# Kernel optimization log

Hardware: AMD Instinct MI355X
Metric: run time of the kernel (lower is better)

The kernel has to match this reference:

```python
import jax, jax.numpy as jnp
import numpy as np

B, N, KNN_K = 4, 4096, 32
C1, C = 128, 256
K_SLOTS, RECON_M, N_RECON = 4, 96, 128
SLOT_ITERS = 3

def _ln(x, g, b):
    m = x.mean(-1, keepdims=True)
    v = jnp.var(x, axis=-1, keepdims=True)
    return (x - m) * jax.lax.rsqrt(v + 1e-5) * g + b

def _gather(f, idx):
    # f [B,P,C], idx [B,N,K] -> [B,N,K,C]
    return jax.vmap(lambda a, i: a[i])(f, idx)

def _knn(xyz, k):
    sq = jnp.sum(xyz * xyz, -1)
    d = sq[:, :, None] + sq[:, None, :] - 2.0 * jnp.einsum('bnc,bmc->bnm', xyz, xyz)
    return jax.lax.top_k(-d, k)[1]

def _conv_block(xyz, feats, W, b):
    # InterZPConv-style: KNN neighbor gather -> per-neighbor transform -> max aggregate
    idx = _knn(xyz, KNN_K)
    rel = _gather(xyz, idx) - xyz[:, :, None, :]
    h = jnp.concatenate([_gather(feats, idx), rel], axis=-1)
    h = jax.nn.relu(jnp.einsum('bnkc,cd->bnkd', h, W) + b)
    return h.max(axis=2)

def _bn(x, g, b):
    # BatchNorm2d (training mode) over (batch, slot) axes for 1x1-conv stacks
    m = x.mean(axis=(0, 1), keepdims=True)
    v = jnp.var(x, axis=(0, 1), keepdims=True)
    return (x - m) * jax.lax.rsqrt(v + 1e-5) * g + b

def _gru(upd, prev, W_ih, W_hh, b_ih, b_hh):
    gi = upd @ W_ih + b_ih
    gh = prev @ W_hh + b_hh
    r = jax.nn.sigmoid(gi[..., :C] + gh[..., :C])
    z = jax.nn.sigmoid(gi[..., C:2 * C] + gh[..., C:2 * C])
    n = jnp.tanh(gi[..., 2 * C:] + r * gh[..., 2 * C:])
    return (1.0 - z) * n + z * prev

def _chamfer(a, b):
    # a [B,M,3], b [B,P,3] -> (min over b per a-point, min over a per b-point), squared dists
    d = jnp.sum((a[..., :, None, :] - b[..., None, :, :]) ** 2, axis=-1)
    return d.min(axis=-1), d.min(axis=-2)

def _fps(pts):
    # farthest point sampling of N_RECON points from pts [P,3]
    P = pts.shape[0]
    d0 = jnp.full((P,), 1e10, pts.dtype)
    def step(carry, _):
        d, last = carry
        d = jnp.minimum(d, jnp.sum((pts - pts[last]) ** 2, axis=-1))
        nxt = jnp.argmax(d).astype(jnp.int32)
        return (d, nxt), nxt
    _, idxs = jax.lax.scan(step, (d0, jnp.array(0, jnp.int32)), None, length=N_RECON - 1)
    return jnp.concatenate([jnp.zeros((1,), jnp.int32), idxs])

def setup_inputs() -> dict:
    key = jax.random.key(0)
    ks = jax.random.split(key, 16)
    w = lambda k, s: jax.random.normal(k, s, jnp.float32) * 0.02
    z = lambda *s: jnp.zeros(s, jnp.float32)
    o = lambda *s: jnp.ones(s, jnp.float32)
    return {
        'x': jax.random.normal(ks[0], (B, 3, N), jnp.float32),
        'pose': jnp.zeros((B, N, 4, 4), jnp.float32),
        'W1': w(ks[1], (1 + 3, C1)), 'b1': z(C1),
        'W2': w(ks[2], (C1 + 3, C)), 'b2': z(C),
        'slots_mu': w(ks[3], (1, 1, C)), 'slots_sigma': jnp.abs(w(ks[4], (1, 1, C))) + 0.01,
        'ln_in_g': o(C), 'ln_in_b': z(C),
        'ln_slot_g': o(C), 'ln_slot_b': z(C),
        'ln_ff_g': o(C), 'ln_ff_b': z(C),
        'Wq': w(ks[5], (C, C)), 'Wk': w(ks[6], (C, C)), 'Wv': w(ks[7], (C, C)),
        'W_ih': w(ks[8], (C, 3 * C)), 'W_hh': w(ks[9], (C, 3 * C)),
        'b_ih': z(3 * C), 'b_hh': z(3 * C),
        'Wm1': w(ks[10], (C, C)), 'bm1': z(C),
        'Wm2': w(ks[11], (C, C)), 'bm2': z(C),
        'Wr1': w(ks[12], (C, C)), 'br1': z(C), 'g1': o(C), 'be1': z(C),
        'Wr2': w(ks[13], (C, C)), 'br2': z(C), 'g2': o(C), 'be2': z(C),
        'Wr3': w(ks[14], (C, RECON_M * 3)), 'br3': z(RECON_M * 3),
    }

def reference(x, pose, W1, b1, W2, b2, slots_mu, slots_sigma, ln_in_g, ln_in_b,
              ln_slot_g, ln_slot_b, ln_ff_g, ln_ff_b, Wq, Wk, Wv,
              W_ih, W_hh, b_ih, b_hh, Wm1, bm1, Wm2, bm2,
              Wr1, br1, g1, be1, Wr2, br2, g2, be2, Wr3, br3):
    xyz = jnp.transpose(x, (0, 2, 1))  # [B,N,3]
    feats = jnp.ones((B, N, 1), x.dtype)  # preprocess_input: unit features, na=1
    f = _conv_block(xyz, feats, W1, b1)   # [B,N,C1]
    f = _conv_block(xyz, f, W2, b2)       # [B,N,C]
    # Slot attention over per-point invariant features
    inp = _ln(f, ln_in_g, ln_in_b)
    kk = inp @ Wk
    vv = inp @ Wv
    slots = slots_mu + slots_sigma * jax.random.normal(jax.random.key(42), (B, K_SLOTS, C), x.dtype)
    scale = C ** -0.5
    attn = None
    for _ in range(SLOT_ITERS):
        prev = slots
        q = _ln(slots, ln_slot_g, ln_slot_b) @ Wq
        logits = scale * jnp.einsum('bkc,bnc->bkn', q, kk)
        attn = jax.nn.softmax(logits, axis=1)  # softmax over slots
        wgt = attn / (attn.sum(axis=-1, keepdims=True) + 1e-8)
        upd = jnp.einsum('bkn,bnc->bkc', wgt, vv)
        slots = _gru(upd, prev, W_ih, W_hh, b_ih, b_hh)
        h = _ln(slots, ln_ff_g, ln_ff_b)
        slots = slots + (jax.nn.relu(h @ Wm1 + bm1) @ Wm2 + bm2)
    attn_out = jnp.transpose(attn, (0, 2, 1))  # [B,N,K] (attn_ori.transpose(1,2))
    # Part reconstruction net (1x1 conv + BN + ReLU stack on slot features)
    h = jax.nn.relu(_bn(slots @ Wr1 + br1, g1, be1))
    h = jax.nn.relu(_bn(h @ Wr2 + br2, g2, be2))
    slot_points = (h @ Wr3 + br3).reshape(B, K_SLOTS, RECON_M, 3)
    all_pts = slot_points.reshape(B, K_SLOTS * RECON_M, 3)
    # FPS downsample + global chamfer against input points
    idx = jax.vmap(_fps)(all_pts)  # [B, N_RECON]
    ds = jnp.take_along_axis(all_pts, idx[..., None], axis=1)  # [B,N_RECON,3]
    d1, d2 = _chamfer(ds, xyz)
    loss = (d1.mean(-1) + d2.mean(-1)).mean()
    return loss, attn_out
```

## Files before the change

### kernel.cpp

```cpp
#include <hip/hip_runtime.h>

#define NBATCH 4
#define NPTS   4096
#define KNNK   32
#define C1D    128
#define CD     256
#define KPAD   160
#define ASTR   168
#define ASTR2  264

typedef _Float16 v8h __attribute__((ext_vector_type(8)));
typedef float    v4f __attribute__((ext_vector_type(4)));
typedef unsigned long long ull;


__device__ __forceinline__ float block_sum256(float v, float* red) {
    #pragma unroll
    for (int o = 32; o; o >>= 1) v += __shfl_down(v, o);
    __syncthreads();
    if ((threadIdx.x & 63) == 0) red[threadIdx.x >> 6] = v;
    __syncthreads();
    return red[0] + red[1] + red[2] + red[3];
}

__device__ __forceinline__ unsigned rotl32(unsigned x, unsigned r) {
    return (x << r) | (x >> (32u - r));
}

__device__ float erfinv_f(float x) {
    float w = -log1pf(-x * x);
    float p;
    if (w < 5.0f) {
        w -= 2.5f;
        p = 2.81022636e-08f;
        p = fmaf(p, w, 3.43273939e-07f);
        p = fmaf(p, w, -3.5233877e-06f);
        p = fmaf(p, w, -4.39150654e-06f);
        p = fmaf(p, w, 0.00021858087f);
        p = fmaf(p, w, -0.00125372503f);
        p = fmaf(p, w, -0.00417768164f);
        p = fmaf(p, w, 0.246640727f);
        p = fmaf(p, w, 1.50140941f);
    } else {
        w = sqrtf(w) - 3.0f;
        p = -0.000200214257f;
        p = fmaf(p, w, 0.000100950558f);
        p = fmaf(p, w, 0.00134934322f);
        p = fmaf(p, w, -0.00367342844f);
        p = fmaf(p, w, 0.00573950773f);
        p = fmaf(p, w, -0.0076224613f);
        p = fmaf(p, w, 0.00943887047f);
        p = fmaf(p, w, 1.00167406f);
        p = fmaf(p, w, 2.83297682f);
    }
    return p * x;
}

__device__ __forceinline__ float bits_to_normal(unsigned bits) {
    unsigned fb = (bits >> 9) | 0x3f800000u;
    float f = __uint_as_float(fb) - 1.0f;
    const float lo = -0.99999994f;
    float u = fmaf(f, 2.0f, lo);
    u = fmaxf(u, lo);
    return 1.41421356237f * erfinv_f(u);
}

__device__ __forceinline__ unsigned fmap(float f) {
    unsigned b = __float_as_uint(f);
    return (b & 0x80000000u) ? ~b : (b | 0x80000000u);
}

template <int CTRL, int RM>
__device__ __forceinline__ ull dpp_min_u64(ull k) {
    unsigned lo = (unsigned)k, hi = (unsigned)(k >> 32);
    unsigned tlo = (unsigned)__builtin_amdgcn_update_dpp((int)lo, (int)lo, CTRL, RM, 0xf, false);
    unsigned thi = (unsigned)__builtin_amdgcn_update_dpp((int)hi, (int)hi, CTRL, RM, 0xf, false);
    ull t = ((ull)thi << 32) | tlo;
    return t < k ? t : k;
}

template <int CTRL, int RM>
__device__ __forceinline__ void dpp_lexmax(float& v, int& ix) {
    int tv = __builtin_amdgcn_update_dpp(__float_as_int(v), __float_as_int(v), CTRL, RM, 0xf, false);
    int ti = __builtin_amdgcn_update_dpp(ix, ix, CTRL, RM, 0xf, false);
    float fv = __int_as_float(tv);
    bool take = (fv > v) || (fv == v && ti < ix);
    v  = take ? fv : v;
    ix = take ? ti : ix;
}


__global__ __launch_bounds__(256) void prep_kernel(const float* __restrict__ x,
                                                   float* __restrict__ xyz,
                                                   float4* __restrict__ xyzw,
                                                   const float* __restrict__ mu,
                                                   const float* __restrict__ sg,
                                                   float* __restrict__ slots,
                                                   float* __restrict__ asum,
                                                   const float* __restrict__ W2,
                                                   const float* __restrict__ Wk,
                                                   const float* __restrict__ Wv,
                                                   _Float16* __restrict__ W2t,
                                                   _Float16* __restrict__ WkvT,
                                                   unsigned* __restrict__ counter) {
    int t = threadIdx.x;
    if (blockIdx.x < 64) {
        int gid = blockIdx.x * 256 + t;
        int b = gid >> 12, n = gid & (NPTS - 1);
        float a0 = x[(b * 3 + 0) * NPTS + n];
        float a1 = x[(b * 3 + 1) * NPTS + n];
        float a2 = x[(b * 3 + 2) * NPTS + n];
        xyz[gid * 3 + 0] = a0; xyz[gid * 3 + 1] = a1; xyz[gid * 3 + 2] = a2;
        float sq = a0 * a0 + a1 * a1 + a2 * a2;
        xyzw[gid] = make_float4(a0, a1, a2, sq);
        if (gid < 16) asum[gid] = 0.0f;
        if (gid == 16) counter[0] = 0u;
        if (gid < 2048) {
            int j = gid;
            unsigned ks0 = 0u, ks1 = 42u, ks2 = 0u ^ 42u ^ 0x1BD11BDAu;
            unsigned x0 = (unsigned)j + ks0;
            unsigned x1 = (unsigned)(j + 2048) + ks1;
            #define RND(r) { x0 += x1; x1 = rotl32(x1, r); x1 ^= x0; }
            RND(13u) RND(15u) RND(26u) RND(6u);  x0 += ks1; x1 += ks2 + 1u;
            RND(17u) RND(29u) RND(16u) RND(24u); x0 += ks2; x1 += ks0 + 2u;
            RND(13u) RND(15u) RND(26u) RND(6u);  x0 += ks0; x1 += ks1 + 3u;
            RND(17u) RND(29u) RND(16u) RND(24u); x0 += ks1; x1 += ks2 + 4u;
            RND(13u) RND(15u) RND(26u) RND(6u);  x0 += ks2; x1 += ks0 + 5u;
            #undef RND
            int c0 = j & 255, c1 = (j + 2048) & 255;
            slots[j]        = mu[c0] + sg[c0] * bits_to_normal(x0);
            slots[j + 2048] = mu[c1] + sg[c1] * bits_to_normal(x1);
        }
    } else if (blockIdx.x < 320) {
        int nb = blockIdx.x - 64;
        if (t < KPAD) W2t[nb * KPAD + t] = (t < 131) ? (_Float16)W2[t * CD + nb] : (_Float16)0.0f;
    } else {
        int n = blockIdx.x - 320;
        float v = (n < 256) ? Wk[t * CD + n] : Wv[t * CD + (n - 256)];
        WkvT[n * CD + t] = (_Float16)v;
    }
}

__global__ __launch_bounds__(256) void knn_kernel(const float4* __restrict__ xyzw,
                                                  int* __restrict__ knn_idx) {
    int wid = threadIdx.x >> 6, lane = threadIdx.x & 63;
    int pid = blockIdx.x * 4 + wid;
    int b = pid >> 12, n = pid & (NPTS - 1);
    const float4* xb = xyzw + (size_t)b * NPTS;
    float4 p = xb[n];
    unsigned d[64];
    #pragma unroll
    for (int i = 0; i < 64; ++i) {
        float4 c = xb[i * 64 + lane];
        float dot = p.x * c.x + p.y * c.y + p.z * c.z;
        d[i] = fmap(p.w + c.w - 2.0f * dot);
    }
    unsigned gv[8]; int gi[8];
    #pragma unroll
    for (int g = 0; g < 8; ++g) {
        unsigned mv = d[g * 8]; int mi = g * 8;
        #pragma unroll
        for (int j = 1; j < 8; ++j)
            if (d[g * 8 + j] < mv) { mv = d[g * 8 + j]; mi = g * 8 + j; }
        gv[g] = mv; gi[g] = mi * 64 + lane;
    }
    unsigned lv = gv[0]; int li = gi[0];
    #pragma unroll
    for (int g = 1; g < 8; ++g)
        if (gv[g] < lv) { lv = gv[g]; li = gi[g]; }

    int* out = knn_idx + (size_t)pid * KNNK;
    #pragma unroll 1
    for (int s = 0; s < KNNK; ++s) {
        ull k = ((ull)lv << 32) | (unsigned)li;
        k = dpp_min_u64<0x111, 0xf>(k);
        k = dpp_min_u64<0x112, 0xf>(k);
        k = dpp_min_u64<0x114, 0xf>(k);
        k = dpp_min_u64<0x118, 0xf>(k);
        k = dpp_min_u64<0x142, 0xa>(k);
        k = dpp_min_u64<0x143, 0xc>(k);
        int fm = __builtin_amdgcn_readlane((int)(unsigned)k, 63);
        if (lane == 0) out[s] = fm;
        int flane = fm & 63;
        int slot  = fm >> 6;
        if (lane == flane) {
            int g = slot >> 3;
            #pragma unroll
            for (int g2 = 0; g2 < 8; ++g2) {
                if (g2 == g) {
                    #pragma unroll
                    for (int j = 0; j < 8; ++j)
                        if (g2 * 8 + j == slot) d[g2 * 8 + j] = 0xFFFFFFFFu;
                    unsigned mv = d[g2 * 8]; int mi = g2 * 8;
                    #pragma unroll
                    for (int j = 1; j < 8; ++j)
                        if (d[g2 * 8 + j] < mv) { mv = d[g2 * 8 + j]; mi = g2 * 8 + j; }
                    gv[g2] = mv; gi[g2] = mi * 64 + lane;
                }
            }
            lv = gv[0]; li = gi[0];
            #pragma unroll
            for (int g2 = 1; g2 < 8; ++g2)
                if (gv[g2] < lv) { lv = gv[g2]; li = gi[g2]; }
        }
    }
}

__global__ __launch_bounds__(128) void conv1_kernel(const float* __restrict__ xyz,
                                                    const int* __restrict__ knn_idx,
                                                    const float* __restrict__ W1,
                                                    const float* __restrict__ b1,
                                                    _Float16* __restrict__ f1h) {
    int pid = blockIdx.x;
    int b = pid >> 12, n = pid & (NPTS - 1);
    int d = threadIdx.x, lane = threadIdx.x & 63;
    const float* xb = xyz + (size_t)b * NPTS * 3;
    float w0 = W1[d], wx = W1[C1D + d], wy = W1[2 * C1D + d], wz = W1[3 * C1D + d];
    float bb = b1[d];
    float px = xb[n * 3], py = xb[n * 3 + 1], pz = xb[n * 3 + 2];
    const int* idx = knn_idx + (size_t)pid * KNNK;
    float cx = 0.0f, cy = 0.0f, cz = 0.0f;
    if (lane < 32) {
        int j = idx[lane];
        cx = xb[j * 3]; cy = xb[j * 3 + 1]; cz = xb[j * 3 + 2];
    }
    float m = -1e30f;
    #pragma unroll
    for (int k = 0; k < KNNK; ++k) {
        float jx = __shfl(cx, k), jy = __shfl(cy, k), jz = __shfl(cz, k);
        float v = w0 + bb + (jx - px) * wx + (jy - py) * wy + (jz - pz) * wz;
        m = fmaxf(m, v);
    }
    f1h[(size_t)pid * C1D + d] = (_Float16)fmaxf(m, 0.0f);
}

__global__ __launch_bounds__(256) void conv2_mfma_kernel(const float* __restrict__ xyz,
                                                         const _Float16* __restrict__ f1h,
                                                         const int* __restrict__ knn_idx,
                                                         const _Float16* __restrict__ W2t,
                                                         const float* __restrict__ b2,
                                                         const float* __restrict__ g_in,
                                                         const float* __restrict__ b_in,
                                                         _Float16* __restrict__ inph) {
    __shared__ _Float16 A[64 * ASTR];
    __shared__ float colmax[2 * CD];
    __shared__ float red[4];
    int pid2 = blockIdx.x;
    int gp0 = pid2 * 2;
    int b = gp0 >> 12, n0 = gp0 & (NPTS - 1);
    int tid = threadIdx.x;
    const int* idx = knn_idx + (size_t)pid2 * 64;
    const float* xb = xyz + (size_t)b * NPTS * 3;

    {
        int r = tid & 63, seg = tid >> 6;
        int j = idx[r];
        const uint4* s4 = (const uint4*)(f1h + ((size_t)b * NPTS + j) * C1D);
        uint4* d4 = (uint4*)&A[r * ASTR];
        #pragma unroll
        for (int i = 0; i < 4; ++i) d4[seg * 4 + i] = s4[seg * 4 + i];
        unsigned* z = (unsigned*)&A[r * ASTR + 128];
        for (int i = seg; i < 20; i += 4) z[i] = 0u;
        int np_ = (r < 32) ? n0 : (n0 + 1);
        if (seg == 0) {
            A[r * ASTR + 128] = (_Float16)(xb[j * 3 + 0] - xb[np_ * 3 + 0]);
            A[r * ASTR + 129] = (_Float16)(xb[j * 3 + 1] - xb[np_ * 3 + 1]);
        } else if (seg == 1) {
            A[r * ASTR + 130] = (_Float16)(xb[j * 3 + 2] - xb[np_ * 3 + 2]);
        }
    }
    __syncthreads();

    int w = tid >> 6, lane = tid & 63, quad = lane >> 4, lr = lane & 15;
    v4f acc[4][4];
    #pragma unroll
    for (int rt = 0; rt < 4; ++rt)
        #pragma unroll
        for (int ct = 0; ct < 4; ++ct)
            acc[rt][ct] = (v4f){0.0f, 0.0f, 0.0f, 0.0f};

    #pragma unroll
    for (int kk = 0; kk < KPAD; kk += 32) {
        v8h af[4], bf[4];
        #pragma unroll
        for (int rt = 0; rt < 4; ++rt)
            af[rt] = *(const v8h*)&A[(rt * 16 + lr) * ASTR + kk + quad * 8];
        #pragma unroll
        for (int ct = 0; ct < 4; ++ct) {
            int ncol = w * 64 + ct * 16 + lr;
            bf[ct] = *(const v8h*)(W2t + (size_t)ncol * KPAD + kk + quad * 8);
        }
        #pragma unroll
        for (int rt = 0; rt < 4; ++rt)
            #pragma unroll
            for (int ct = 0; ct < 4; ++ct)
                acc[rt][ct] = __builtin_amdgcn_mfma_f32_16x16x32_f16(af[rt], bf[ct], acc[rt][ct], 0, 0, 0);
    }

    #pragma unroll
    for (int ct = 0; ct < 4; ++ct) {
        float tm[4];
        #pragma unroll
        for (int rt = 0; rt < 4; ++rt) {
            v4f a = acc[rt][ct];
            float v = fmaxf(fmaxf(a[0], a[1]), fmaxf(a[2], a[3]));
            v = fmaxf(v, __shfl_xor(v, 16));
            v = fmaxf(v, __shfl_xor(v, 32));
            tm[rt] = v;
        }
        float p0 = fmaxf(tm[0], tm[1]);
        float p1 = fmaxf(tm[2], tm[3]);
        if (quad == 0) {
            colmax[0 * CD + w * 64 + ct * 16 + lr] = p0;
            colmax[1 * CD + w * 64 + ct * 16 + lr] = p1;
        }
    }
    __syncthreads();

    int d = tid;
    #pragma unroll
    for (int p = 0; p < 2; ++p) {
        float v = fmaxf(colmax[p * CD + d] + b2[d], 0.0f);
        float s = block_sum256(v, red);
        float mean = s * (1.0f / 256.0f);
        float s2 = block_sum256(v * v, red);
        float var = s2 * (1.0f / 256.0f) - mean * mean;
        float iv = (v - mean) * rsqrtf(var + 1e-5f) * g_in[d] + b_in[d];
        inph[(size_t)(gp0 + p) * CD + d] = (_Float16)iv;
    }
}

__global__ __launch_bounds__(256) void kv_mfma_kernel(const _Float16* __restrict__ inph,
                                                      const _Float16* __restrict__ WkvT,
                                                      float* __restrict__ kk,
                                                      float* __restrict__ vv,
                                                      const float* __restrict__ slots,
                                                      const float* __restrict__ g_sl,
                                                      const float* __restrict__ b_sl,
                                                      const float* __restrict__ Wq,
                                                      float* __restrict__ qb) {
    __shared__ _Float16 A[64 * ASTR2];
    __shared__ float sl[CD];
    __shared__ float red[4];
    int tid = threadIdx.x;
    if (blockIdx.x >= 512) {
        int row = blockIdx.x - 512;
        int d = tid;
        float v = slots[row * CD + d];
        float s = block_sum256(v, red);
        float mean = s * (1.0f / 256.0f);
        float s2 = block_sum256(v * v, red);
        float var = s2 * (1.0f / 256.0f) - mean * mean;
        float ln = (v - mean) * rsqrtf(var + 1e-5f) * g_sl[d] + b_sl[d];
        sl[d] = ln;
        __syncthreads();
        float acc = 0.0f;
        const float4* sp = (const float4*)sl;
        for (int c4 = 0; c4 < 64; ++c4) {
            float4 x = sp[c4];
            int cb = c4 * 4;
            acc += x.x * Wq[cb * CD + d] + x.y * Wq[(cb + 1) * CD + d]
                 + x.z * Wq[(cb + 2) * CD + d] + x.w * Wq[(cb + 3) * CD + d];
        }
        qb[row * CD + d] = acc;
        return;
    }
    int rb = blockIdx.x >> 1, half = blockIdx.x & 1;
    int row0 = rb * 64;
    {
        const uint4* src4 = (const uint4*)(inph + (size_t)row0 * CD);
        #pragma unroll
        for (int i = 0; i < 8; ++i) {
            int idx = i * 256 + tid;
            int row = idx >> 5, c8 = idx & 31;
            *(uint4*)&A[row * ASTR2 + c8 * 8] = src4[idx];
        }
    }
    __syncthreads();
    int w = tid >> 6, lane = tid & 63, quad = lane >> 4, lr = lane & 15;
    v4f acc[4][4];
    #pragma unroll
    for (int rt = 0; rt < 4; ++rt)
        #pragma unroll
        for (int ct = 0; ct < 4; ++ct)
            acc[rt][ct] = (v4f){0.0f, 0.0f, 0.0f, 0.0f};
    #pragma unroll
    for (int ks = 0; ks < CD; ks += 32) {
        v8h af[4], bf[4];
        #pragma unroll
        for (int rt = 0; rt < 4; ++rt)
            af[rt] = *(const v8h*)&A[(rt * 16 + lr) * ASTR2 + ks + quad * 8];
        #pragma unroll
        for (int ct = 0; ct < 4; ++ct) {
            int ncol = half * 256 + w * 64 + ct * 16 + lr;
            bf[ct] = *(const v8h*)(WkvT + (size_t)ncol * CD + ks + quad * 8);
        }
        #pragma unroll
        for (int rt = 0; rt < 4; ++rt)
            #pragma unroll
            for (int ct = 0; ct < 4; ++ct)
                acc[rt][ct] = __builtin_amdgcn_mfma_f32_16x16x32_f16(af[rt], bf[ct], acc[rt][ct], 0, 0, 0);
    }
    float* dst = half ? vv : kk;
    #pragma unroll
    for (int rt = 0; rt < 4; ++rt)
        #pragma unroll
        for (int ct = 0; ct < 4; ++ct) {
            int col = w * 64 + ct * 16 + lr;
            #pragma unroll
            for (int r = 0; r < 4; ++r) {
                int row = rt * 16 + quad * 4 + r;
                dst[(size_t)(row0 + row) * CD + col] = acc[rt][ct][r];
            }
        }
}

__global__ __launch_bounds__(256) void attn_updp_kernel(const float* __restrict__ q,
                                                        const float* __restrict__ kk,
                                                        const float* __restrict__ vv,
                                                        float* __restrict__ asum,
                                                        float* __restrict__ updp,
                                                        float* __restrict__ out_attn) {
    int b = blockIdx.x >> 6;
    int chunk = blockIdx.x & 63;
    int t = threadIdx.x;
    __shared__ float qs[4 * CD];
    __shared__ float logit[64 * 4];
    __shared__ float aw[64 * 4];
    for (int i = t; i < 4 * CD; i += 256) qs[i] = q[b * 4 * CD + i];
    __syncthreads();

    int p = t & 63, r = t >> 6;
    int n = chunk * 64 + p;
    {
        const float4* kp = (const float4*)(kk + ((size_t)b * NPTS + n) * CD);
        const float4* qr = (const float4*)(qs + r * CD);
        float a = 0.0f;
        for (int c4 = 0; c4 < 64; ++c4) {
            float4 kv = kp[c4];
            float4 x = qr[c4];
            a += kv.x * x.x + kv.y * x.y + kv.z * x.z + kv.w * x.w;
        }
        logit[p * 4 + r] = 0.0625f * a;
    }
    __syncthreads();
    if (t < 64) {
        float l0 = logit[t * 4 + 0], l1 = logit[t * 4 + 1];
        float l2 = logit[t * 4 + 2], l3 = logit[t * 4 + 3];
        float mx = fmaxf(fmaxf(l0, l1), fmaxf(l2, l3));
        float e0 = expf(l0 - mx), e1 = expf(l1 - mx), e2 = expf(l2 - mx), e3 = expf(l3 - mx);
        float inv = 1.0f / (e0 + e1 + e2 + e3);
        e0 *= inv; e1 *= inv; e2 *= inv; e3 *= inv;
        aw[t * 4 + 0] = e0; aw[t * 4 + 1] = e1; aw[t * 4 + 2] = e2; aw[t * 4 + 3] = e3;
        if (out_attn) {
            float* o = out_attn + ((size_t)b * NPTS + chunk * 64 + t) * 4;
            o[0] = e0; o[1] = e1; o[2] = e2; o[3] = e3;
        }
        float s0 = e0, s1 = e1, s2 = e2, s3 = e3;
        #pragma unroll
        for (int o = 32; o; o >>= 1) {
            s0 += __shfl_down(s0, o); s1 += __shfl_down(s1, o);
            s2 += __shfl_down(s2, o); s3 += __shfl_down(s3, o);
        }
        if (t == 0) {
            atomicAdd(&asum[b * 4 + 0], s0);
            atomicAdd(&asum[b * 4 + 1], s1);
            atomicAdd(&asum[b * 4 + 2], s2);
            atomicAdd(&asum[b * 4 + 3], s3);
        }
    }
    __syncthreads();

    float ac0 = 0.0f, ac1 = 0.0f, ac2 = 0.0f, ac3 = 0.0f;
    const float* vb = vv + ((size_t)b * NPTS + chunk * 64) * CD;
    for (int nn2 = 0; nn2 < 64; ++nn2) {
        float v = vb[(size_t)nn2 * CD + t];
        float4 w4 = *(const float4*)&aw[nn2 * 4];
        ac0 += w4.x * v; ac1 += w4.y * v; ac2 += w4.z * v; ac3 += w4.w * v;
    }
    updp[((size_t)(b * 4 + 0) * 64 + chunk) * CD + t] = ac0;
    updp[((size_t)(b * 4 + 1) * 64 + chunk) * CD + t] = ac1;
    updp[((size_t)(b * 4 + 2) * 64 + chunk) * CD + t] = ac2;
    updp[((size_t)(b * 4 + 3) * 64 + chunk) * CD + t] = ac3;
}

__global__ __launch_bounds__(256) void gru_gates_kernel(const float* __restrict__ updp,
                                                        const float* __restrict__ asum,
                                                        const float* __restrict__ slots,
                                                        const float* __restrict__ W_ih,
                                                        const float* __restrict__ W_hh,
                                                        const float* __restrict__ b_ih,
                                                        const float* __restrict__ b_hh,
                                                        float* __restrict__ gi,
                                                        float* __restrict__ gh) {
    int idx = blockIdx.x;
    int row = idx / 6, rem = idx % 6;
    int gate = rem >> 1, half = rem & 1;
    int d = threadIdx.x;
    __shared__ float su[CD], sp[CD];
    float f = 1.0f / (asum[row] + 1e-8f);
    float u = 0.0f;
    for (int p = 0; p < 64; ++p) u += updp[((size_t)row * 64 + p) * CD + d];
    u *= f;
    su[d] = u; sp[d] = slots[row * CD + d];
    __syncthreads();
    float acc_i = half ? 0.0f : b_ih[gate * CD + d];
    float acc_h = half ? 0.0f : b_hh[gate * CD + d];
    const float* wi = W_ih + gate * CD + d;
    const float* wh = W_hh + gate * CD + d;
    int c0 = half * 128;
    for (int c = c0; c < c0 + 128; ++c) {
        acc_i += su[c] * wi[c * 3 * CD];
        acc_h += sp[c] * wh[c * 3 * CD];
    }
    gi[((size_t)(row * 3 + gate) * 2 + half) * CD + d] = acc_i;
    gh[((size_t)(row * 3 + gate) * 2 + half) * CD + d] = acc_h;
}

__global__ __launch_bounds__(256) void gru_mlp_kernel(const float* __restrict__ gi,
                                                      const float* __restrict__ gh,
                                                      float* __restrict__ slots,
                                                      const float* __restrict__ g_ff,
                                                      const float* __restrict__ b_ff,
                                                      const float* __restrict__ Wm1,
                                                      const float* __restrict__ bm1,
                                                      const float* __restrict__ Wm2,
                                                      const float* __restrict__ bm2,
                                                      float* __restrict__ asum,
                                                      const float* __restrict__ g_sl,
                                                      const float* __restrict__ b_sl,
                                                      const float* __restrict__ Wq,
                                                      float* __restrict__ qv) {
    int row = blockIdx.x;
    int d = threadIdx.x;
    __shared__ float sh[CD];
    __shared__ float red[4];
    float prev = slots[row * CD + d];
    float gir = gi[((size_t)(row * 3 + 0) * 2 + 0) * CD + d] + gi[((size_t)(row * 3 + 0) * 2 + 1) * CD + d];
    float giz = gi[((size_t)(row * 3 + 1) * 2 + 0) * CD + d] + gi[((size_t)(row * 3 + 1) * 2 + 1) * CD + d];
    float gin = gi[((size_t)(row * 3 + 2) * 2 + 0) * CD + d] + gi[((size_t)(row * 3 + 2) * 2 + 1) * CD + d];
    float ghr = gh[((size_t)(row * 3 + 0) * 2 + 0) * CD + d] + gh[((size_t)(row * 3 + 0) * 2 + 1) * CD + d];
    float ghz = gh[((size_t)(row * 3 + 1) * 2 + 0) * CD + d] + gh[((size_t)(row * 3 + 1) * 2 + 1) * CD + d];
    float ghn = gh[((size_t)(row * 3 + 2) * 2 + 0) * CD + d] + gh[((size_t)(row * 3 + 2) * 2 + 1) * CD + d];
    if (d == 0) asum[row] = 0.0f;
    float r = 1.0f / (1.0f + expf(-(gir + ghr)));
    float z = 1.0f / (1.0f + expf(-(giz + ghz)));
    float nn = tanhf(gin + r * ghn);
    float sNew = (1.0f - z) * nn + z * prev;
    float s = block_sum256(sNew, red);
    float mean = s * (1.0f / 256.0f);
    float s2 = block_sum256(sNew * sNew, red);
    float var = s2 * (1.0f / 256.0f) - mean * mean;
    float h = (sNew - mean) * rsqrtf(var + 1e-5f) * g_ff[d] + b_ff[d];
    __syncthreads();
    sh[d] = h;
    __syncthreads();
    float y = bm1[d];
    {
        const float4* hp = (const float4*)sh;
        for (int c4 = 0; c4 < 64; ++c4) {
            float4 x = hp[c4];
            int cb = c4 * 4;
            y += x.x * Wm1[cb * CD + d] + x.y * Wm1[(cb + 1) * CD + d]
               + x.z * Wm1[(cb + 2) * CD + d] + x.w * Wm1[(cb + 3) * CD + d];
        }
    }
    y = fmaxf(y, 0.0f);
    __syncthreads();
    sh[d] = y;
    __syncthreads();
    float o = bm2[d];
    {
        const float4* hp = (const float4*)sh;
        for (int c4 = 0; c4 < 64; ++c4) {
            float4 x = hp[c4];
            int cb = c4 * 4;
            o += x.x * Wm2[cb * CD + d] + x.y * Wm2[(cb + 1) * CD + d]
               + x.z * Wm2[(cb + 2) * CD + d] + x.w * Wm2[(cb + 3) * CD + d];
        }
    }
    float fin = sNew + o;
    slots[row * CD + d] = fin;
    if (qv) {
        float v = fin;
        float s3 = block_sum256(v, red);
        float mean2 = s3 * (1.0f / 256.0f);
        float s4 = block_sum256(v * v, red);
        float var2 = s4 * (1.0f / 256.0f) - mean2 * mean2;
        float ln = (v - mean2) * rsqrtf(var2 + 1e-5f) * g_sl[d] + b_sl[d];
        __syncthreads();
        sh[d] = ln;
        __syncthreads();
        float acc = 0.0f;
        const float4* sp = (const float4*)sh;
        for (int c4 = 0; c4 < 64; ++c4) {
            float4 x = sp[c4];
            int cb = c4 * 4;
            acc += x.x * Wq[cb * CD + d] + x.y * Wq[(cb + 1) * CD + d]
                 + x.z * Wq[(cb + 2) * CD + d] + x.w * Wq[(cb + 3) * CD + d];
        }
        qv[row * CD + d] = acc;
    }
}

__global__ __launch_bounds__(256) void recon_layer_kernel(const float* __restrict__ in,
                                                          const float* __restrict__ W,
                                                          const float* __restrict__ bias,
                                                          const float* __restrict__ g,
                                                          const float* __restrict__ be,
                                                          float* __restrict__ outb) {
    __shared__ float sin[16 * CD];
    __shared__ float tb[16 * 16];
    int t = threadIdx.x;
    for (int i = t; i < 16 * CD; i += 256) sin[i] = in[i];
    __syncthreads();
    int col = t & 15, row = t >> 4;
    int colg = blockIdx.x * 16 + col;
    float acc = bias[colg];
    for (int c4 = 0; c4 < 64; ++c4) {
        int cb = c4 * 4;
        float w0 = W[cb * CD + colg], w1 = W[(cb + 1) * CD + colg];
        float w2 = W[(cb + 2) * CD + colg], w3 = W[(cb + 3) * CD + colg];
        float4 x = *(const float4*)(sin + row * CD + cb);
        acc += x.x * w0 + x.y * w1 + x.z * w2 + x.w * w3;
    }
    tb[row * 16 + col] = acc;
    __syncthreads();
    float mean = 0.0f;
    for (int r = 0; r < 16; ++r) mean += tb[r * 16 + col];
    mean *= (1.0f / 16.0f);
    float var = 0.0f;
    for (int r = 0; r < 16; ++r) { float dd = tb[r * 16 + col] - mean; var += dd * dd; }
    var *= (1.0f / 16.0f);
    float inv = rsqrtf(var + 1e-5f);
    outb[row * CD + colg] = fmaxf(0.0f, (acc - mean) * inv * g[colg] + be[colg]);
}

__global__ __launch_bounds__(320) void recon3_fps_kernel(const float* __restrict__ h2g,
                                                         const float* __restrict__ Wr3,
                                                         const float* __restrict__ br3,
                                                         float* __restrict__ spts,
                                                         int* __restrict__ fidx,
                                                         float* __restrict__ lacc,
                                                         unsigned* __restrict__ mnbuf) {
    __shared__ float h2[16 * CD];
    __shared__ float sp[384 * 3];
    int b = blockIdx.x;
    int d = threadIdx.x;
    for (int i = d; i < 16 * CD; i += 320) h2[i] = h2g[i];
    __syncthreads();
    if (d < 288) {
        float t4[4];
        #pragma unroll
        for (int rl = 0; rl < 4; ++rl) t4[rl] = br3[d];
        for (int c4 = 0; c4 < 64; ++c4) {
            int cb = c4 * 4;
            float w0 = Wr3[cb * 288 + d], w1 = Wr3[(cb + 1) * 288 + d];
            float w2 = Wr3[(cb + 2) * 288 + d], w3 = Wr3[(cb + 3) * 288 + d];
            #pragma unroll
            for (int rl = 0; rl < 4; ++rl) {
                float4 x = *(const float4*)(h2 + (b * 4 + rl) * CD + cb);
                t4[rl] += x.x * w0 + x.y * w1 + x.z * w2 + x.w * w3;
            }
        }
        #pragma unroll
        for (int rl = 0; rl < 4; ++rl) {
            spts[(b * 4 + rl) * 288 + d] = t4[rl];
            sp[rl * 288 + d] = t4[rl];
        }
    }
    __syncthreads();

    if (d < 64) {
        int lane = d;
        int* out = fidx + b * 128;
        if (lane == 0) out[0] = 0;
        if (b == 0 && lane == 0) lacc[0] = 0.0f;
        mnbuf[b * 128 + lane] = 0x7F800000u;
        mnbuf[b * 128 + 64 + lane] = 0x7F800000u;
        float px[6], py[6], pz[6], dd[6];
        #pragma unroll
        for (int i = 0; i < 6; ++i) {
            int m = i * 64 + lane;
            px[i] = sp[m * 3]; py[i] = sp[m * 3 + 1]; pz[i] = sp[m * 3 + 2];
            dd[i] = 1e10f;
        }
        float lx = sp[0], ly = sp[1], lz = sp[2];
        #pragma unroll 1
        for (int s = 1; s < 128; ++s) {
            #pragma unroll
            for (int i = 0; i < 6; ++i) {
                float dx = px[i] - lx, dy = py[i] - ly, dz = pz[i] - lz;
                dd[i] = fminf(dd[i], dx * dx + dy * dy + dz * dz);
            }
            float bv = dd[0]; int bi = lane;
            #pragma unroll
            for (int i = 1; i < 6; ++i)
                if (dd[i] > bv) { bv = dd[i]; bi = i * 64 + lane; }
            dpp_lexmax<0x111, 0xf>(bv, bi);
            dpp_lexmax<0x112, 0xf>(bv, bi);
            dpp_lexmax<0x114, 0xf>(bv, bi);
            dpp_lexmax<0x118, 0xf>(bv, bi);
            dpp_lexmax<0x142, 0xa>(bv, bi);
            dpp_lexmax<0x143, 0xc>(bv, bi);
            int fm = __builtin_amdgcn_readlane(bi, 63);
            if (lane == 0) out[s] = fm;
            int slot = fm >> 6, sl_lane = fm & 63;
            float sx = px[0], sy = py[0], sz = pz[0];
            #pragma unroll
            for (int i = 1; i < 6; ++i)
                if (slot == i) { sx = px[i]; sy = py[i]; sz = pz[i]; }
            lx = __int_as_float(__builtin_amdgcn_readlane(__float_as_int(sx), sl_lane));
            ly = __int_as_float(__builtin_amdgcn_readlane(__float_as_int(sy), sl_lane));
            lz = __int_as_float(__builtin_amdgcn_readlane(__float_as_int(sz), sl_lane));
        }
    }
}

__global__ __launch_bounds__(256) void chamfer_kernel(const float* __restrict__ spts,
                                                      const int* __restrict__ fidx,
                                                      const float* __restrict__ xyz,
                                                      float* __restrict__ lacc,
                                                      unsigned* __restrict__ mnbuf,
                                                      unsigned* __restrict__ counter,
                                                      float* __restrict__ out) {
    int t = threadIdx.x;
    __shared__ float ds[128 * 3];
    __shared__ float tile[256 * 3];
    __shared__ float red[4];
    __shared__ unsigned done;
    if (blockIdx.x < 64) {
        int b = blockIdx.x >> 4, chunk = blockIdx.x & 15;
        const float* pts = spts + (size_t)b * 384 * 3;
        if (t < 128) {
            int j = fidx[b * 128 + t];
            ds[t * 3] = pts[j * 3]; ds[t * 3 + 1] = pts[j * 3 + 1]; ds[t * 3 + 2] = pts[j * 3 + 2];
        }
        __syncthreads();
        int n = chunk * 256 + t;
        const float* xb = xyz + (size_t)b * NPTS * 3;
        float px = xb[n * 3], py = xb[n * 3 + 1], pz = xb[n * 3 + 2];
        float mn = 1e30f;
        #pragma unroll 4
        for (int jj = 0; jj < 128; ++jj) {
            float dx = ds[jj * 3] - px, dy = ds[jj * 3 + 1] - py, dz = ds[jj * 3 + 2] - pz;
            mn = fminf(mn, dx * dx + dy * dy + dz * dz);
        }
        float total = block_sum256(mn * (1.0f / 4096.0f), red);
        if (t == 0) atomicAdd(lacc, total);
    } else {
        int bid = blockIdx.x - 64;
        int b = bid >> 4, chunk = bid & 15;
        const float* xb = xyz + ((size_t)b * NPTS + chunk * 256) * 3;
        for (int i = t; i < 768; i += 256) tile[i] = xb[i];
        __syncthreads();
        if (t < 128) {
            int j = fidx[b * 128 + t];
            const float* pts = spts + (size_t)b * 384 * 3;
            float px = pts[j * 3], py = pts[j * 3 + 1], pz = pts[j * 3 + 2];
            float mn = 1e30f;
            #pragma unroll 4
            for (int i = 0; i < 256; ++i) {
                float dx = tile[i * 3] - px, dy = tile[i * 3 + 1] - py, dz = tile[i * 3 + 2] - pz;
                mn = fminf(mn, dx * dx + dy * dy + dz * dz);
            }
            atomicMin(&mnbuf[b * 128 + t], __float_as_uint(mn));
        }
    }
    __threadfence();
    __syncthreads();
    if (t == 0) done = atomicAdd(counter, 1u);
    __syncthreads();
    if (done == 127u) {
        unsigned a0 = atomicAdd(&mnbuf[t], 0u);
        unsigned a1 = atomicAdd(&mnbuf[t + 256], 0u);
        float v = (__uint_as_float(a0) + __uint_as_float(a1)) * (1.0f / 128.0f);
        __syncthreads();
        float tot = block_sum256(v, red);
        if (t == 0) {
            float l = atomicAdd(lacc, 0.0f);
            out[0] = (l + tot) * 0.25f;
        }
    }
}


extern "C" void kernel_launch(void* const* d_in, const int* in_sizes, int n_in,
                              void* d_out, int out_size, void* d_ws, size_t ws_size,
                              hipStream_t stream) {
    (void)in_sizes; (void)n_in; (void)out_size; (void)ws_size;
    const float* x    = (const float*)d_in[0];
    const float* W1   = (const float*)d_in[2];
    const float* b1   = (const float*)d_in[3];
    const float* W2   = (const float*)d_in[4];
    const float* b2   = (const float*)d_in[5];
    const float* mu   = (const float*)d_in[6];
    const float* sg   = (const float*)d_in[7];
    const float* g_in = (const float*)d_in[8];
    const float* b_in = (const float*)d_in[9];
    const float* g_sl = (const float*)d_in[10];
    const float* b_sl = (const float*)d_in[11];
    const float* g_ff = (const float*)d_in[12];
    const float* b_ff = (const float*)d_in[13];
    const float* Wq   = (const float*)d_in[14];
    const float* Wk   = (const float*)d_in[15];
    const float* Wv   = (const float*)d_in[16];
    const float* W_ih = (const float*)d_in[17];
    const float* W_hh = (const float*)d_in[18];
    const float* b_ih = (const float*)d_in[19];
    const float* b_hh = (const float*)d_in[20];
    const float* Wm1  = (const float*)d_in[21];
    const float* bm1  = (const float*)d_in[22];
    const float* Wm2  = (const float*)d_in[23];
    const float* bm2  = (const float*)d_in[24];
    const float* Wr1  = (const float*)d_in[25];
    const float* br1  = (const float*)d_in[26];
    const float* g1   = (const float*)d_in[27];
    const float* be1  = (const float*)d_in[28];
    const float* Wr2  = (const float*)d_in[29];
    const float* br2  = (const float*)d_in[30];
    const float* g2   = (const float*)d_in[31];
    const float* be2  = (const float*)d_in[32];
    const float* Wr3  = (const float*)d_in[33];
    const float* br3  = (const float*)d_in[34];

    float* ws    = (float*)d_ws;
    float* xyz   = ws;
    float* xyzw  = xyz + 49152;
    int*   knn   = (int*)(xyzw + 65536);
    _Float16* f1h = (_Float16*)(knn + 524288);
    _Float16* W2t = (_Float16*)((float*)f1h + 1048576);
    _Float16* WkvT = (_Float16*)((float*)W2t + 20480);
    _Float16* inph = (_Float16*)((float*)WkvT + 65536);
    float* kkb   = (float*)inph + 2097152;
    float* vvb   = kkb + 4194304;
    float* slots = vvb + 4194304;
    float* qb    = slots + 4096;
    float* asum  = qb + 4096;
    float* updp  = asum + 16;
    float* gi    = updp + 262144;
    float* gh    = gi + 24576;
    float* h1g   = gh + 24576;
    float* h2g   = h1g + 4096;
    float* spts  = h2g + 4096;
    int*   fidx  = (int*)(spts + 4608);
    float* lacc  = (float*)(fidx + 512);
    unsigned* mnbuf = (unsigned*)(lacc + 1);
    unsigned* counter = mnbuf + 512;

    float* out = (float*)d_out;

    prep_kernel<<<832, 256, 0, stream>>>(x, xyz, (float4*)xyzw, mu, sg, slots, asum,
                                         W2, Wk, Wv, W2t, WkvT, counter);
    knn_kernel<<<NBATCH * NPTS / 4, 256, 0, stream>>>((const float4*)xyzw, knn);
    conv1_kernel<<<NBATCH * NPTS, 128, 0, stream>>>(xyz, knn, W1, b1, f1h);
    conv2_mfma_kernel<<<NBATCH * NPTS / 2, 256, 0, stream>>>(xyz, f1h, knn, W2t, b2, g_in, b_in, inph);
    kv_mfma_kernel<<<NBATCH * NPTS / 64 * 2 + 16, 256, 0, stream>>>(inph, WkvT, kkb, vvb,
                                                                    slots, g_sl, b_sl, Wq, qb);

    for (int it = 0; it < 3; ++it) {
        attn_updp_kernel<<<256, 256, 0, stream>>>(qb, kkb, vvb, asum, updp,
                                                  (it == 2) ? (out + 1) : (float*)nullptr);
        gru_gates_kernel<<<96, 256, 0, stream>>>(updp, asum, slots, W_ih, W_hh, b_ih, b_hh, gi, gh);
        gru_mlp_kernel<<<16, 256, 0, stream>>>(gi, gh, slots, g_ff, b_ff, Wm1, bm1, Wm2, bm2, asum,
                                               g_sl, b_sl, Wq, (it < 2) ? qb : (float*)nullptr);
    }

    recon_layer_kernel<<<16, 256, 0, stream>>>(slots, Wr1, br1, g1, be1, h1g);
    recon_layer_kernel<<<16, 256, 0, stream>>>(h1g, Wr2, br2, g2, be2, h2g);
    recon3_fps_kernel<<<4, 320, 0, stream>>>(h2g, Wr3, br3, spts, fidx, lacc, mnbuf);
    chamfer_kernel<<<128, 256, 0, stream>>>(spts, fidx, xyz, lacc, mnbuf, counter, out);
}
```

Baseline: 669.9 us.

## Fuse GRU gates and MLP kernels via last-block-done atomic counter

Merges the GRU gate kernel and the GRU/MLP/Q-projection kernel into one launch. Each of the six blocks per slot row computes its share of the gates, fences, and bumps a per-row atomic counter. The last block to finish reads the gate partials with device-scope loads and runs the GRU update, layer norm, MLP and Q projection. This removes three kernel launches per run in exchange for atomic traffic and a serialized tail on the last-arriving block.

```diff
diff --git a/kernel.cpp b/kernel.cpp
--- a/kernel.cpp
+++ b/kernel.cpp
@@ -89,6 +89,10 @@
     ix = take ? ti : ix;
 }
 
+__device__ __forceinline__ float dev_load(const float* p) {
+    return __hip_atomic_load(p, __ATOMIC_RELAXED, __HIP_MEMORY_SCOPE_AGENT);
+}
+
 
 __global__ __launch_bounds__(256) void prep_kernel(const float* __restrict__ x,
                                                    float* __restrict__ xyz,
@@ -102,7 +106,8 @@
                                                    const float* __restrict__ Wv,
                                                    _Float16* __restrict__ W2t,
                                                    _Float16* __restrict__ WkvT,
-                                                   unsigned* __restrict__ counter) {
+                                                   unsigned* __restrict__ counter,
+                                                   unsigned* __restrict__ rowcnt) {
     int t = threadIdx.x;
     if (blockIdx.x < 64) {
         int gid = blockIdx.x * 256 + t;
@@ -115,6 +120,7 @@
         xyzw[gid] = make_float4(a0, a1, a2, sq);
         if (gid < 16) asum[gid] = 0.0f;
         if (gid == 16) counter[0] = 0u;
+        if (gid >= 32 && gid < 48) rowcnt[gid - 32] = 0u;
         if (gid < 2048) {
             int j = gid;
             unsigned ks0 = 0u, ks1 = 42u, ks2 = 0u ^ 42u ^ 0x1BD11BDAu;
@@ -484,69 +490,74 @@
     updp[((size_t)(b * 4 + 3) * 64 + chunk) * CD + t] = ac3;
 }
 
-__global__ __launch_bounds__(256) void gru_gates_kernel(const float* __restrict__ updp,
-                                                        const float* __restrict__ asum,
-                                                        const float* __restrict__ slots,
-                                                        const float* __restrict__ W_ih,
-                                                        const float* __restrict__ W_hh,
-                                                        const float* __restrict__ b_ih,
-                                                        const float* __restrict__ b_hh,
-                                                        float* __restrict__ gi,
-                                                        float* __restrict__ gh) {
+__global__ __launch_bounds__(256) void gru_gates_mlp_kernel(const float* __restrict__ updp,
+                                                            float* __restrict__ asum,
+                                                            float* __restrict__ slots,
+                                                            const float* __restrict__ W_ih,
+                                                            const float* __restrict__ W_hh,
+                                                            const float* __restrict__ b_ih,
+                                                            const float* __restrict__ b_hh,
+                                                            float* __restrict__ gi,
+                                                            float* __restrict__ gh,
+                                                            const float* __restrict__ g_ff,
+                                                            const float* __restrict__ b_ff,
+                                                            const float* __restrict__ Wm1,
+                                                            const float* __restrict__ bm1,
+                                                            const float* __restrict__ Wm2,
+                                                            const float* __restrict__ bm2,
+                                                            const float* __restrict__ g_sl,
+                                                            const float* __restrict__ b_sl,
+                                                            const float* __restrict__ Wq,
+                                                            float* __restrict__ qv,
+                                                            unsigned* __restrict__ rowcnt) {
     int idx = blockIdx.x;
     int row = idx / 6, rem = idx % 6;
     int gate = rem >> 1, half = rem & 1;
-    int d = threadIdx.x;
+    int t = threadIdx.x;
+    int d = t;
     __shared__ float su[CD], sp[CD];
-    float f = 1.0f / (asum[row] + 1e-8f);
-    float u = 0.0f;
-    for (int p = 0; p < 64; ++p) u += updp[((size_t)row * 64 + p) * CD + d];
-    u *= f;
-    su[d] = u; sp[d] = slots[row * CD + d];
-    __syncthreads();
-    float acc_i = half ? 0.0f : b_ih[gate * CD + d];
-    float acc_h = half ? 0.0f : b_hh[gate * CD + d];
-    const float* wi = W_ih + gate * CD + d;
-    const float* wh = W_hh + gate * CD + d;
-    int c0 = half * 128;
-    for (int c = c0; c < c0 + 128; ++c) {
-        acc_i += su[c] * wi[c * 3 * CD];
-        acc_h += sp[c] * wh[c * 3 * CD];
-    }
-    gi[((size_t)(row * 3 + gate) * 2 + half) * CD + d] = acc_i;
-    gh[((size_t)(row * 3 + gate) * 2 + half) * CD + d] = acc_h;
-}
-
-__global__ __launch_bounds__(256) void gru_mlp_kernel(const float* __restrict__ gi,
-                                                      const float* __restrict__ gh,
-                                                      float* __restrict__ slots,
-                                                      const float* __restrict__ g_ff,
-                                                      const float* __restrict__ b_ff,
-                                                      const float* __restrict__ Wm1,
-                                                      const float* __restrict__ bm1,
-                                                      const float* __restrict__ Wm2,
-                                                      const float* __restrict__ bm2,
-                                                      float* __restrict__ asum,
-                                                      const float* __restrict__ g_sl,
-                                                      const float* __restrict__ b_sl,
-                                                      const float* __restrict__ Wq,
-                                                      float* __restrict__ qv) {
-    int row = blockIdx.x;
-    int d = threadIdx.x;
-    __shared__ float sh[CD];
     __shared__ float red[4];
+    __shared__ unsigned done;
+    {
+        float f = 1.0f / (asum[row] + 1e-8f);
+        float u = 0.0f;
+        for (int p = 0; p < 64; ++p) u += updp[((size_t)row * 64 + p) * CD + d];
+        u *= f;
+        su[d] = u; sp[d] = slots[row * CD + d];
+        __syncthreads();
+        float acc_i = half ? 0.0f : b_ih[gate * CD + d];
+        float acc_h = half ? 0.0f : b_hh[gate * CD + d];
+        const float* wi = W_ih + gate * CD + d;
+        const float* wh = W_hh + gate * CD + d;
+        int c0 = half * 128;
+        for (int c = c0; c < c0 + 128; ++c) {
+            acc_i += su[c] * wi[c * 3 * CD];
+            acc_h += sp[c] * wh[c * 3 * CD];
+        }
+        gi[((size_t)(row * 3 + gate) * 2 + half) * CD + d] = acc_i;
+        gh[((size_t)(row * 3 + gate) * 2 + half) * CD + d] = acc_h;
+    }
+    __threadfence();
+    __syncthreads();
+    if (t == 0) done = atomicAdd(&rowcnt[row], 1u);
+    __syncthreads();
+    if (done != 5u) return;
+    if (t == 0) atomicExch(&rowcnt[row], 0u);
+
+    float* sh = su;
     float prev = slots[row * CD + d];
-    float gir = gi[((size_t)(row * 3 + 0) * 2 + 0) * CD + d] + gi[((size_t)(row * 3 + 0) * 2 + 1) * CD + d];
-    float giz = gi[((size_t)(row * 3 + 1) * 2 + 0) * CD + d] + gi[((size_t)(row * 3 + 1) * 2 + 1) * CD + d];
-    float gin = gi[((size_t)(row * 3 + 2) * 2 + 0) * CD + d] + gi[((size_t)(row * 3 + 2) * 2 + 1) * CD + d];
-    float ghr = gh[((size_t)(row * 3 + 0) * 2 + 0) * CD + d] + gh[((size_t)(row * 3 + 0) * 2 + 1) * CD + d];
-    float ghz = gh[((size_t)(row * 3 + 1) * 2 + 0) * CD + d] + gh[((size_t)(row * 3 + 1) * 2 + 1) * CD + d];
-    float ghn = gh[((size_t)(row * 3 + 2) * 2 + 0) * CD + d] + gh[((size_t)(row * 3 + 2) * 2 + 1) * CD + d];
+    float gir = dev_load(&gi[((size_t)(row * 3 + 0) * 2 + 0) * CD + d]) + dev_load(&gi[((size_t)(row * 3 + 0) * 2 + 1) * CD + d]);
+    float giz = dev_load(&gi[((size_t)(row * 3 + 1) * 2 + 0) * CD + d]) + dev_load(&gi[((size_t)(row * 3 + 1) * 2 + 1) * CD + d]);
+    float gin = dev_load(&gi[((size_t)(row * 3 + 2) * 2 + 0) * CD + d]) + dev_load(&gi[((size_t)(row * 3 + 2) * 2 + 1) * CD + d]);
+    float ghr = dev_load(&gh[((size_t)(row * 3 + 0) * 2 + 0) * CD + d]) + dev_load(&gh[((size_t)(row * 3 + 0) * 2 + 1) * CD + d]);
+    float ghz = dev_load(&gh[((size_t)(row * 3 + 1) * 2 + 0) * CD + d]) + dev_load(&gh[((size_t)(row * 3 + 1) * 2 + 1) * CD + d]);
+    float ghn = dev_load(&gh[((size_t)(row * 3 + 2) * 2 + 0) * CD + d]) + dev_load(&gh[((size_t)(row * 3 + 2) * 2 + 1) * CD + d]);
     if (d == 0) asum[row] = 0.0f;
     float r = 1.0f / (1.0f + expf(-(gir + ghr)));
     float z = 1.0f / (1.0f + expf(-(giz + ghz)));
     float nn = tanhf(gin + r * ghn);
     float sNew = (1.0f - z) * nn + z * prev;
+    __syncthreads();
     float s = block_sum256(sNew, red);
     float mean = s * (1.0f / 256.0f);
     float s2 = block_sum256(sNew * sNew, red);
@@ -592,9 +603,9 @@
         sh[d] = ln;
         __syncthreads();
         float acc = 0.0f;
-        const float4* sp = (const float4*)sh;
+        const float4* sp2 = (const float4*)sh;
         for (int c4 = 0; c4 < 64; ++c4) {
-            float4 x = sp[c4];
+            float4 x = sp2[c4];
             int cb = c4 * 4;
             acc += x.x * Wq[cb * CD + d] + x.y * Wq[(cb + 1) * CD + d]
                  + x.z * Wq[(cb + 2) * CD + d] + x.w * Wq[(cb + 3) * CD + d];
@@ -847,11 +858,12 @@
     float* lacc  = (float*)(fidx + 512);
     unsigned* mnbuf = (unsigned*)(lacc + 1);
     unsigned* counter = mnbuf + 512;
+    unsigned* rowcnt  = counter + 1;
 
     float* out = (float*)d_out;
 
     prep_kernel<<<832, 256, 0, stream>>>(x, xyz, (float4*)xyzw, mu, sg, slots, asum,
-                                         W2, Wk, Wv, W2t, WkvT, counter);
+                                         W2, Wk, Wv, W2t, WkvT, counter, rowcnt);
     knn_kernel<<<NBATCH * NPTS / 4, 256, 0, stream>>>((const float4*)xyzw, knn);
     conv1_kernel<<<NBATCH * NPTS, 128, 0, stream>>>(xyz, knn, W1, b1, f1h);
     conv2_mfma_kernel<<<NBATCH * NPTS / 2, 256, 0, stream>>>(xyz, f1h, knn, W2t, b2, g_in, b_in, inph);
@@ -861,9 +873,10 @@
     for (int it = 0; it < 3; ++it) {
         attn_updp_kernel<<<256, 256, 0, stream>>>(qb, kkb, vvb, asum, updp,
                                                   (it == 2) ? (out + 1) : (float*)nullptr);
-        gru_gates_kernel<<<96, 256, 0, stream>>>(updp, asum, slots, W_ih, W_hh, b_ih, b_hh, gi, gh);
-        gru_mlp_kernel<<<16, 256, 0, stream>>>(gi, gh, slots, g_ff, b_ff, Wm1, bm1, Wm2, bm2, asum,
-                                               g_sl, b_sl, Wq, (it < 2) ? qb : (float*)nullptr);
+        gru_gates_mlp_kernel<<<96, 256, 0, stream>>>(updp, asum, slots, W_ih, W_hh, b_ih, b_hh,
+                                                     gi, gh, g_ff, b_ff, Wm1, bm1, Wm2, bm2,
+                                                     g_sl, b_sl, Wq, (it < 2) ? qb : (float*)nullptr,
+                                                     rowcnt);
     }
 
     recon_layer_kernel<<<16, 256, 0, stream>>>(slots, Wr1, br1, g1, be1, h1g);
```

Measured after the change: 679.3 us. About the same (+1.4%).
